# Optimization experiments

Hardware: AMD Instinct MI355X
Metric: run time of the kernel (lower is better)

## Reference

```python
import jax, jax.numpy as jnp
import numpy as np

B, S, NN = 16, 512, 8          # batch, spatial nodes, neighbors per node
IN, H, NHEAD = 128, 512, 4     # input_size, hidden_size, n_head


def _forward(inputs, h, c, h_spatial, a_src, w_fg, b_fg, w_ig, b_ig,
             w_ih, w_hh, b_ih, b_hh):
    N = B * S
    x = inputs.reshape(N, IN)
    h = h.reshape(N, H)
    c = c.reshape(N, H)
    hs = h_spatial.reshape(N, NN, H)

    # attention logits: concat(h, neighbor) @ a_src, split to avoid materializing concat
    a_self, a_nb = a_src[:H], a_src[H:]              # [H, NHEAD] each
    attn = h @ a_self                                  # [N, NHEAD]
    attn = attn[:, None, :] + jnp.einsum('nkh,hm->nkm', hs, a_nb)  # [N, NN, NHEAD]
    attn = jnp.where(attn >= 0, attn, 0.2 * attn)      # leaky_relu(0.2)
    attn = jax.nn.softmax(attn, axis=1)                # softmax over neighbors

    # aggregate neighbors per head -> [N, NHEAD*H]
    agg = jnp.einsum('nkm,nkh->nmh', attn, hs).reshape(N, NHEAD * H)

    spatial_f = jax.nn.sigmoid(agg @ w_fg.T + b_fg)    # [N, H]
    spatial_i = jax.nn.sigmoid(agg @ w_ig.T + b_ig)
    h = h * spatial_i
    c = c * spatial_f

    # torch LSTMCell: gate order i, f, g, o
    gates = x @ w_ih.T + b_ih + h @ w_hh.T + b_hh      # [N, 4H]
    i_g, f_g, g_g, o_g = jnp.split(gates, 4, axis=1)
    i_g = jax.nn.sigmoid(i_g)
    f_g = jax.nn.sigmoid(f_g)
    g_g = jnp.tanh(g_g)
    o_g = jax.nn.sigmoid(o_g)
    c_new = f_g * c + i_g * g_g
    h_new = o_g * jnp.tanh(c_new)
    return h_new.reshape(B, S, H), c_new.reshape(B, S, H)


def setup_inputs() -> dict:
    key = jax.random.key(0)
    ks = jax.random.split(key, 16)
    xav = lambda k, shp: jax.random.uniform(
        k, shp, jnp.float32, -1.0, 1.0) * np.sqrt(6.0 / (shp[0] + shp[1]))
    return {
        'inputs': jax.random.normal(ks[0], (B, S, IN), jnp.float32),
        'h': jax.random.normal(ks[1], (B, S, H), jnp.float32),
        'c': jax.random.normal(ks[2], (B, S, H), jnp.float32),
        'h_spatial': jax.random.normal(ks[3], (B, S, NN, H), jnp.float32),
        'a_src': xav(ks[4], (2 * H, NHEAD)),
        'w_fg': jax.random.normal(ks[5], (H, NHEAD * H), jnp.float32) * 0.02,
        'b_fg': jnp.zeros((H,), jnp.float32),
        'w_ig': jax.random.normal(ks[6], (H, NHEAD * H), jnp.float32) * 0.02,
        'b_ig': jnp.zeros((H,), jnp.float32),
        'w_ih': jax.random.normal(ks[7], (4 * H, IN), jnp.float32) * 0.02,
        'w_hh': jax.random.normal(ks[8], (4 * H, H), jnp.float32) * 0.02,
        'b_ih': jnp.zeros((4 * H,), jnp.float32),
        'b_hh': jnp.zeros((4 * H,), jnp.float32),
    }


def reference(inputs, h, c, h_spatial, a_src, w_fg, b_fg, w_ig, b_ig,
              w_ih, w_hh, b_ih, b_hh):
    return _forward(inputs, h, c, h_spatial, a_src, w_fg, b_fg, w_ig, b_ig,
                    w_ih, w_hh, b_ih, b_hh)
```

## Files before the change

### kernel.cpp

```cpp
#include <hip/hip_runtime.h>
#include <hip/hip_bf16.h>
#include <cstdint>
#include <cstddef>

#define N_ROWS 8192
#define HDIM 512
#define INDIM 128
#define NHEADS 4
#define NNB 8

typedef __bf16 bf16_t;
typedef __bf16 bf16x8 __attribute__((ext_vector_type(8)));
typedef __bf16 bf16x4 __attribute__((ext_vector_type(4)));
typedef __bf16 bf16x2 __attribute__((ext_vector_type(2)));
typedef float f32x4 __attribute__((ext_vector_type(4)));

__device__ __forceinline__ float sigmoidf_(float x) { return 1.0f / (1.0f + expf(-x)); }

__device__ __forceinline__ void load_lds16(const void* g, void* l) {
  __builtin_amdgcn_global_load_lds(
      (const __attribute__((address_space(1))) void*)g,
      (__attribute__((address_space(3))) void*)l, 16, 0, 0);
}

__global__ __launch_bounds__(256) void pack_kernel(
    const float* __restrict__ w_fg, const float* __restrict__ w_ig,
    const float* __restrict__ w_ih, const float* __restrict__ w_hh,
    const float* __restrict__ b_ih, const float* __restrict__ b_hh,
    const float* __restrict__ x,
    bf16_t* __restrict__ W1, bf16_t* __restrict__ W2i,
    float* __restrict__ b2, bf16_t* __restrict__ A2)
{
  int idx = blockIdx.x * 256 + threadIdx.x;
  if (idx < 524288) {
    const int e = idx * 4, r = e >> 11, k = e & 2047;
    const float* src = (r < 512) ? &w_fg[(size_t)r * 2048 + k]
                                 : &w_ig[(size_t)(r - 512) * 2048 + k];
    const float4 v = *(const float4*)src;
    bf16x4 o; o[0] = (bf16_t)v.x; o[1] = (bf16_t)v.y; o[2] = (bf16_t)v.z; o[3] = (bf16_t)v.w;
    *(bf16x4*)&W1[e] = o;
    return;
  }
  idx -= 524288;
  if (idx < 327680) {
    const int e = idx * 4, r = e / 640, k = e - r * 640;
    const int rp = (r & 511) * 4 + (r >> 9);
    const float* src = (k < 128) ? &w_ih[(size_t)r * 128 + k]
                                 : &w_hh[(size_t)r * 512 + (k - 128)];
    const float4 v = *(const float4*)src;
    bf16x4 o; o[0] = (bf16_t)v.x; o[1] = (bf16_t)v.y; o[2] = (bf16_t)v.z; o[3] = (bf16_t)v.w;
    *(bf16x4*)&W2i[(size_t)rp * 640 + k] = o;
    return;
  }
  idx -= 327680;
  if (idx < 2048) {
    const int q = idx >> 2, g = idx & 3;
    b2[idx] = b_ih[g * 512 + q] + b_hh[g * 512 + q];
    return;
  }
  idx -= 2048;
  if (idx < 262144) {
    const int e = idx * 4, n = e >> 7, cc = e & 127;
    const float4 v = *(const float4*)&x[e];
    bf16x4 o; o[0] = (bf16_t)v.x; o[1] = (bf16_t)v.y; o[2] = (bf16_t)v.z; o[3] = (bf16_t)v.w;
    *(bf16x4*)&A2[(size_t)n * 640 + cc] = o;
  }
}

__global__ __launch_bounds__(256) void attn_agg_kernel(
    const float* __restrict__ h, const float* __restrict__ hs,
    const float* __restrict__ a_src, bf16_t* __restrict__ agg)
{
  __shared__ float s_hs[NNB][HDIM];
  __shared__ float s_h[HDIM];
  __shared__ float s_logit[NNB][NHEADS];
  __shared__ float s_self[NHEADS];

  const int n = blockIdx.x;
  const int t = threadIdx.x;
  const float* hs_n = hs + (size_t)n * (NNB * HDIM);
  const float* h_n  = h  + (size_t)n * HDIM;

  {
    const float4* s4 = (const float4*)hs_n;
    float4* d4 = (float4*)&s_hs[0][0];
#pragma unroll
    for (int i = 0; i < 4; ++i) d4[t + i * 256] = s4[t + i * 256];
    if (t < HDIM / 4) ((float4*)s_h)[t] = ((const float4*)h_n)[t];
  }
  __syncthreads();

  const int wave = t >> 6, lane = t & 63;
#pragma unroll
  for (int kk = 0; kk < 2; ++kk) {
    const int k = wave * 2 + kk;
    float acc0 = 0.f, acc1 = 0.f, acc2 = 0.f, acc3 = 0.f;
#pragma unroll
    for (int i = 0; i < HDIM / 64; ++i) {
      const int hh = i * 64 + lane;
      const float v = s_hs[k][hh];
      const float4 av = *(const float4*)(a_src + (size_t)(HDIM + hh) * NHEADS);
      acc0 += v * av.x; acc1 += v * av.y; acc2 += v * av.z; acc3 += v * av.w;
    }
    float accs[NHEADS] = {acc0, acc1, acc2, acc3};
#pragma unroll
    for (int m = 0; m < NHEADS; ++m) {
      float a = accs[m];
#pragma unroll
      for (int off = 32; off > 0; off >>= 1) a += __shfl_xor(a, off);
      if (lane == 0) s_logit[k][m] = a;
    }
  }
  if (wave == 0) {
    float acc0 = 0.f, acc1 = 0.f, acc2 = 0.f, acc3 = 0.f;
#pragma unroll
    for (int i = 0; i < HDIM / 64; ++i) {
      const int hh = i * 64 + lane;
      const float v = s_h[hh];
      const float4 av = *(const float4*)(a_src + (size_t)hh * NHEADS);
      acc0 += v * av.x; acc1 += v * av.y; acc2 += v * av.z; acc3 += v * av.w;
    }
    float accs[NHEADS] = {acc0, acc1, acc2, acc3};
#pragma unroll
    for (int m = 0; m < NHEADS; ++m) {
      float a = accs[m];
#pragma unroll
      for (int off = 32; off > 0; off >>= 1) a += __shfl_xor(a, off);
      if (lane == 0) s_self[m] = a;
    }
  }
  __syncthreads();

  float w[NNB][NHEADS];
#pragma unroll
  for (int m = 0; m < NHEADS; ++m) {
    const float sm = s_self[m];
    float mx = -1e30f;
#pragma unroll
    for (int k = 0; k < NNB; ++k) {
      float l = sm + s_logit[k][m];
      l = (l >= 0.f) ? l : 0.2f * l;
      w[k][m] = l;
      mx = fmaxf(mx, l);
    }
    float sum = 0.f;
#pragma unroll
    for (int k = 0; k < NNB; ++k) { const float e = expf(w[k][m] - mx); w[k][m] = e; sum += e; }
    const float inv = 1.f / sum;
#pragma unroll
    for (int k = 0; k < NNB; ++k) w[k][m] *= inv;
  }

  bf16_t* agg_n = agg + (size_t)n * (NHEADS * HDIM);
  const int hh = t * 2;
  float e0[NNB], e1[NNB];
#pragma unroll
  for (int k = 0; k < NNB; ++k) { e0[k] = s_hs[k][hh]; e1[k] = s_hs[k][hh + 1]; }
#pragma unroll
  for (int m = 0; m < NHEADS; ++m) {
    float a0 = 0.f, a1 = 0.f;
#pragma unroll
    for (int k = 0; k < NNB; ++k) { a0 += w[k][m] * e0[k]; a1 += w[k][m] * e1[k]; }
    bf16x2 pk; pk[0] = (bf16_t)a0; pk[1] = (bf16_t)a1;
    *(bf16x2*)(agg_n + m * HDIM + hh) = pk;
  }
}

__global__ __launch_bounds__(256) void gemm1_kernel(
    const bf16_t* __restrict__ A, const bf16_t* __restrict__ Bt,
    const float* __restrict__ b_fg, const float* __restrict__ b_ig,
    const float* __restrict__ c_in, const float* __restrict__ h_in,
    float* __restrict__ cprime, bf16_t* __restrict__ A2)
{
  __shared__ bf16_t At[128][64];
  __shared__ bf16_t Bs[64][64];

  const int tid  = threadIdx.x;
  const int wave = tid >> 6, lane = tid & 63;
  const int wr = wave >> 1, wc = wave & 1;
  const int bm0 = blockIdx.x * 128;
  const int bn0 = blockIdx.y * 64;
  const int K = 2048;

  f32x4 acc[4][2] = {};

  const int srow = tid >> 3;
  const int sch  = tid & 7;
  const int gsw8 = (sch ^ (srow & 7)) * 8;
  const int sch8 = sch * 8;
  const int frow = lane & 15;
  const int fq   = lane >> 4;

  for (int k0 = 0; k0 < K; k0 += 64) {
#pragma unroll
    for (int r = 0; r < 4; ++r)
      load_lds16(A + (size_t)(bm0 + r * 32 + srow) * K + k0 + gsw8,
                 &At[r * 32 + srow][sch8]);
#pragma unroll
    for (int r = 0; r < 2; ++r)
      load_lds16(Bt + (size_t)(bn0 + r * 32 + srow) * K + k0 + gsw8,
                 &Bs[r * 32 + srow][sch8]);
    __syncthreads();

#pragma unroll
    for (int kk = 0; kk < 2; ++kk) {
      const int fro8 = ((kk * 4 + fq) ^ (frow & 7)) * 8;
      bf16x8 af[4], bv[2];
#pragma unroll
      for (int i = 0; i < 4; ++i)
        af[i] = *(const bf16x8*)&At[wr * 64 + i * 16 + frow][fro8];
#pragma unroll
      for (int j = 0; j < 2; ++j)
        bv[j] = *(const bf16x8*)&Bs[wc * 32 + j * 16 + frow][fro8];
#pragma unroll
      for (int i = 0; i < 4; ++i)
#pragma unroll
        for (int j = 0; j < 2; ++j)
          acc[i][j] = __builtin_amdgcn_mfma_f32_16x16x32_bf16(af[i], bv[j], acc[i][j], 0, 0, 0);
    }
    __syncthreads();
  }

  const int col_in = lane & 15;
  const int row_in = (lane >> 4) * 4;
#pragma unroll
  for (int i = 0; i < 4; ++i) {
#pragma unroll
    for (int j = 0; j < 2; ++j) {
      const int col = bn0 + wc * 32 + j * 16 + col_in;
#pragma unroll
      for (int r = 0; r < 4; ++r) {
        const int row = bm0 + wr * 64 + i * 16 + row_in + r;
        const float v = acc[i][j][r];
        if (col < 512) {
          const float s = sigmoidf_(v + b_fg[col]);
          cprime[(size_t)row * 512 + col] = c_in[(size_t)row * 512 + col] * s;
        } else {
          const int jj = col - 512;
          const float s = sigmoidf_(v + b_ig[jj]);
          A2[(size_t)row * 640 + 128 + jj] = (bf16_t)(h_in[(size_t)row * 512 + jj] * s);
        }
      }
    }
  }
}

__global__ __launch_bounds__(256) void gemm2_kernel(
    const bf16_t* __restrict__ A, const bf16_t* __restrict__ Bt,
    const float* __restrict__ b2, const float* __restrict__ cprime,
    float* __restrict__ out)
{
  __shared__ union {
    struct { bf16_t A[128][64]; bf16_t B[128][64]; } st;
    float epi[64][128];
  } sm;

  const int tid  = threadIdx.x;
  const int wave = tid >> 6, lane = tid & 63;
  const int wr = wave >> 1, wc = wave & 1;
  const int bm0 = blockIdx.x * 128;
  const int bn0 = blockIdx.y * 128;
  const int K = 640;

  f32x4 acc[4][4] = {};

  const int srow = tid >> 3;
  const int sch  = tid & 7;
  const int gsw8 = (sch ^ (srow & 7)) * 8;
  const int sch8 = sch * 8;
  const int frow = lane & 15;
  const int fq   = lane >> 4;

  for (int k0 = 0; k0 < K; k0 += 64) {
#pragma unroll
    for (int r = 0; r < 4; ++r)
      load_lds16(A + (size_t)(bm0 + r * 32 + srow) * K + k0 + gsw8,
                 &sm.st.A[r * 32 + srow][sch8]);
#pragma unroll
    for (int r = 0; r < 4; ++r)
      load_lds16(Bt + (size_t)(bn0 + r * 32 + srow) * K + k0 + gsw8,
                 &sm.st.B[r * 32 + srow][sch8]);
    __syncthreads();

#pragma unroll
    for (int kk = 0; kk < 2; ++kk) {
      const int fro8 = ((kk * 4 + fq) ^ (frow & 7)) * 8;
      bf16x8 af[4], bv[4];
#pragma unroll
      for (int i = 0; i < 4; ++i)
        af[i] = *(const bf16x8*)&sm.st.A[wr * 64 + i * 16 + frow][fro8];
#pragma unroll
      for (int j = 0; j < 4; ++j)
        bv[j] = *(const bf16x8*)&sm.st.B[wc * 64 + j * 16 + frow][fro8];
#pragma unroll
      for (int i = 0; i < 4; ++i)
#pragma unroll
        for (int j = 0; j < 4; ++j)
          acc[i][j] = __builtin_amdgcn_mfma_f32_16x16x32_bf16(af[i], bv[j], acc[i][j], 0, 0, 0);
    }
    __syncthreads();
  }

  const int col_in = lane & 15;
  const int row_in = (lane >> 4) * 4;
  const int q0i = bn0 >> 2;
  const int qi  = tid & 31;
  const int r0  = tid >> 5;

#pragma unroll
  for (int p = 0; p < 2; ++p) {
    if (wr == p) {
#pragma unroll
      for (int i = 0; i < 4; ++i)
#pragma unroll
        for (int j = 0; j < 4; ++j)
#pragma unroll
          for (int r = 0; r < 4; ++r)
            sm.epi[i * 16 + row_in + r][wc * 64 + j * 16 + col_in] = acc[i][j][r];
    }
    __syncthreads();
    const float4 bb = *(const float4*)&b2[(size_t)(q0i + qi) * 4];
#pragma unroll
    for (int rr = 0; rr < 8; ++rr) {
      const int lr = r0 + rr * 8;
      const float4 g4 = *(const float4*)&sm.epi[lr][qi * 4];
      const int grow = bm0 + p * 64 + lr;
      const int q    = q0i + qi;
      const float cp = cprime[(size_t)grow * 512 + q];
      const float ig = sigmoidf_(g4.x + bb.x);
      const float fg = sigmoidf_(g4.y + bb.y);
      const float gg = tanhf(g4.z + bb.z);
      const float og = sigmoidf_(g4.w + bb.w);
      const float cn = fg * cp + ig * gg;
      const float hn = og * tanhf(cn);
      out[(size_t)grow * 512 + q] = hn;
      out[(size_t)N_ROWS * 512 + (size_t)grow * 512 + q] = cn;
    }
    __syncthreads();
  }
}

extern "C" void kernel_launch(void* const* d_in, const int* in_sizes, int n_in,
                              void* d_out, int out_size, void* d_ws, size_t ws_size,
                              hipStream_t stream) {
  const float* x     = (const float*)d_in[0];
  const float* h     = (const float*)d_in[1];
  const float* c     = (const float*)d_in[2];
  const float* hsp   = (const float*)d_in[3];
  const float* a_src = (const float*)d_in[4];
  const float* w_fg  = (const float*)d_in[5];
  const float* b_fg  = (const float*)d_in[6];
  const float* w_ig  = (const float*)d_in[7];
  const float* b_ig  = (const float*)d_in[8];
  const float* w_ih  = (const float*)d_in[9];
  const float* w_hh  = (const float*)d_in[10];
  const float* b_ih  = (const float*)d_in[11];
  const float* b_hh  = (const float*)d_in[12];
  float* out = (float*)d_out;

  uint8_t* ws = (uint8_t*)d_ws;
  bf16_t* agg    = (bf16_t*)(ws);
  bf16_t* W1     = (bf16_t*)(ws + 33554432);
  bf16_t* W2i    = (bf16_t*)(ws + 37748736);
  float*  b2     = (float*) (ws + 40370176);
  bf16_t* A2     = (bf16_t*)(ws + 40378368);
  float*  cprime = (float*) (ws + 50864128);

  pack_kernel<<<4360, 256, 0, stream>>>(w_fg, w_ig, w_ih, w_hh, b_ih, b_hh, x,
                                        W1, W2i, b2, A2);
  attn_agg_kernel<<<N_ROWS, 256, 0, stream>>>(h, hsp, a_src, agg);
  gemm1_kernel<<<dim3(64, 16), 256, 0, stream>>>(
      agg, W1, b_fg, b_ig, c, h, cprime, A2);
  gemm2_kernel<<<dim3(64, 16), 256, 0, stream>>>(
      A2, W2i, b2, cprime, out);
}
```

Baseline: 186.2 us.

## Enlarge gemm1 tiles and add triple-buffered async LDS pipeline

Rewrites gemm1 to use 256x128 block tiles with 512 threads (8 waves) and a three-stage LDS ring buffer filled by global_load_lds. Loads for tile t+2 are split across the two k-halves and issued while the current tile is computed, with explicit vmcnt waits and barriers replacing the two syncthreads per iteration. MFMA sections are given raised wave priority. The aim is to hide global-load latency and raise data reuse per block. In exchange it uses far more LDS (about 144KB per block) and more registers, and the grid drops to 256 blocks, which roughly matches the CU count.

```diff
diff --git a/kernel.cpp b/kernel.cpp
--- a/kernel.cpp
+++ b/kernel.cpp
@@ -166,23 +166,24 @@
   }
 }
 
-__global__ __launch_bounds__(256) void gemm1_kernel(
+__global__ __launch_bounds__(512, 2) void gemm1_kernel(
     const bf16_t* __restrict__ A, const bf16_t* __restrict__ Bt,
     const float* __restrict__ b_fg, const float* __restrict__ b_ig,
     const float* __restrict__ c_in, const float* __restrict__ h_in,
     float* __restrict__ cprime, bf16_t* __restrict__ A2)
 {
-  __shared__ bf16_t At[128][64];
-  __shared__ bf16_t Bs[64][64];
+  __shared__ bf16_t At[3][256][64];
+  __shared__ bf16_t Bs[3][128][64];
 
   const int tid  = threadIdx.x;
-  const int wave = tid >> 6, lane = tid & 63;
-  const int wr = wave >> 1, wc = wave & 1;
-  const int bm0 = blockIdx.x * 128;
-  const int bn0 = blockIdx.y * 64;
+  const int lane = tid & 63;
+  const int wave = tid >> 6;
+  const int wr = wave >> 2, wc = wave & 3;
+  const int bm0 = blockIdx.x * 256;
+  const int bn0 = blockIdx.y * 128;
   const int K = 2048;
 
-  f32x4 acc[4][2] = {};
+  f32x4 acc[8][2] = {};
 
   const int srow = tid >> 3;
   const int sch  = tid & 7;
@@ -191,46 +192,75 @@
   const int frow = lane & 15;
   const int fq   = lane >> 4;
 
-  for (int k0 = 0; k0 < K; k0 += 64) {
-#pragma unroll
-    for (int r = 0; r < 4; ++r)
-      load_lds16(A + (size_t)(bm0 + r * 32 + srow) * K + k0 + gsw8,
-                 &At[r * 32 + srow][sch8]);
+  auto STAGE_A3 = [&](int buf, int k0) {
+#pragma unroll
+    for (int r = 0; r < 3; ++r)
+      load_lds16(A + (size_t)(bm0 + r * 64 + srow) * K + k0 + gsw8,
+                 &At[buf][r * 64 + srow][sch8]);
+  };
+  auto STAGE_B3 = [&](int buf, int k0) {
+    load_lds16(A + (size_t)(bm0 + 192 + srow) * K + k0 + gsw8,
+               &At[buf][192 + srow][sch8]);
 #pragma unroll
     for (int r = 0; r < 2; ++r)
-      load_lds16(Bt + (size_t)(bn0 + r * 32 + srow) * K + k0 + gsw8,
-                 &Bs[r * 32 + srow][sch8]);
-    __syncthreads();
-
-#pragma unroll
-    for (int kk = 0; kk < 2; ++kk) {
-      const int fro8 = ((kk * 4 + fq) ^ (frow & 7)) * 8;
-      bf16x8 af[4], bv[2];
-#pragma unroll
-      for (int i = 0; i < 4; ++i)
-        af[i] = *(const bf16x8*)&At[wr * 64 + i * 16 + frow][fro8];
+      load_lds16(Bt + (size_t)(bn0 + r * 64 + srow) * K + k0 + gsw8,
+                 &Bs[buf][r * 64 + srow][sch8]);
+  };
+  auto COMPUTE = [&](int buf, int kk) {
+    const int fro8 = ((kk * 4 + fq) ^ (frow & 7)) * 8;
+    bf16x8 af[8], bv[2];
+#pragma unroll
+    for (int i = 0; i < 8; ++i)
+      af[i] = *(const bf16x8*)&At[buf][wr * 128 + i * 16 + frow][fro8];
+#pragma unroll
+    for (int j = 0; j < 2; ++j)
+      bv[j] = *(const bf16x8*)&Bs[buf][wc * 32 + j * 16 + frow][fro8];
+    __builtin_amdgcn_s_setprio(1);
+#pragma unroll
+    for (int i = 0; i < 8; ++i)
 #pragma unroll
       for (int j = 0; j < 2; ++j)
-        bv[j] = *(const bf16x8*)&Bs[wc * 32 + j * 16 + frow][fro8];
-#pragma unroll
-      for (int i = 0; i < 4; ++i)
-#pragma unroll
-        for (int j = 0; j < 2; ++j)
-          acc[i][j] = __builtin_amdgcn_mfma_f32_16x16x32_bf16(af[i], bv[j], acc[i][j], 0, 0, 0);
-    }
-    __syncthreads();
+        acc[i][j] = __builtin_amdgcn_mfma_f32_16x16x32_bf16(af[i], bv[j], acc[i][j], 0, 0, 0);
+    __builtin_amdgcn_s_setprio(0);
+  };
+
+  const int nt = K >> 6;
+  STAGE_A3(0, 0);   STAGE_B3(0, 0);
+  STAGE_A3(1, 64);  STAGE_B3(1, 64);
+  asm volatile("s_waitcnt vmcnt(6)" ::: "memory");
+  __builtin_amdgcn_s_barrier();
+  __builtin_amdgcn_sched_barrier(0);
+
+  for (int t = 0; t < nt; ++t) {
+    const int buf  = t % 3;
+    const int nb   = (t + 2) % 3;
+    const bool more = (t + 2) < nt;
+    if (more) STAGE_A3(nb, (t + 2) * 64);
+    COMPUTE(buf, 0);
+    __builtin_amdgcn_sched_barrier(0);
+    __builtin_amdgcn_s_barrier();
+    __builtin_amdgcn_sched_barrier(0);
+    if (more) STAGE_B3(nb, (t + 2) * 64);
+    COMPUTE(buf, 1);
+    if (t + 1 < nt) {
+      __builtin_amdgcn_sched_barrier(0);
+      if (more) asm volatile("s_waitcnt vmcnt(6)" ::: "memory");
+      else      asm volatile("s_waitcnt vmcnt(0)" ::: "memory");
+      __builtin_amdgcn_s_barrier();
+      __builtin_amdgcn_sched_barrier(0);
+    }
   }
 
   const int col_in = lane & 15;
   const int row_in = (lane >> 4) * 4;
 #pragma unroll
-  for (int i = 0; i < 4; ++i) {
+  for (int i = 0; i < 8; ++i) {
 #pragma unroll
     for (int j = 0; j < 2; ++j) {
       const int col = bn0 + wc * 32 + j * 16 + col_in;
 #pragma unroll
       for (int r = 0; r < 4; ++r) {
-        const int row = bm0 + wr * 64 + i * 16 + row_in + r;
+        const int row = bm0 + wr * 128 + i * 16 + row_in + r;
         const float v = acc[i][j][r];
         if (col < 512) {
           const float s = sigmoidf_(v + b_fg[col]);
@@ -369,7 +399,7 @@
   pack_kernel<<<4360, 256, 0, stream>>>(w_fg, w_ig, w_ih, w_hh, b_ih, b_hh, x,
                                         W1, W2i, b2, A2);
   attn_agg_kernel<<<N_ROWS, 256, 0, stream>>>(h, hsp, a_src, agg);
-  gemm1_kernel<<<dim3(64, 16), 256, 0, stream>>>(
+  gemm1_kernel<<<dim3(32, 8), 512, 0, stream>>>(
       agg, W1, b_fg, b_ig, c, h, cprime, A2);
   gemm2_kernel<<<dim3(64, 16), 256, 0, stream>>>(
       A2, W2i, b2, cprime, out);
```

After: 214.5 us. +15.2%, slower.
